# Optimization experiments

Hardware: AMD Instinct MI355X
Metric: run time of the kernel (lower is better)

The kernel has to match this reference:

```python
import jax, jax.numpy as jnp
import numpy as np

IN_FEATURES = 4096
OUT_FEATURES = 11008
GROUP_SIZE = 64
NUM_GROUPS = (OUT_FEATURES * IN_FEATURES) // GROUP_SIZE  # 704512, no padding


def setup_inputs() -> dict:
    key = jax.random.key(0)
    k_x, k_q, k_s, k_m, k_b = jax.random.split(key, 5)
    x = jax.random.normal(k_x, (2, 2048, IN_FEATURES), dtype=jnp.float32)
    weight_q3 = jax.random.randint(k_q, (NUM_GROUPS, GROUP_SIZE), 0, 8, dtype=jnp.int32)
    # positive scales, matching clamp(min=1e-8) in the quantizer
    weight_scales = jax.random.uniform(k_s, (NUM_GROUPS,), dtype=jnp.float32, minval=0.01, maxval=1.0)
    weight_sparse_mask = jax.random.uniform(k_m, (NUM_GROUPS, GROUP_SIZE)) < 0.1
    bias = jax.random.normal(k_b, (OUT_FEATURES,), dtype=jnp.float32)
    return {"x": x, "weight_q3": weight_q3, "weight_scales": weight_scales,
            "weight_sparse_mask": weight_sparse_mask, "bias": bias}


def _dequant(weight_q3, weight_scales, weight_sparse_mask):
    # x_norm = q/7; deq = x_norm*2*s - s = (2*q/7 - 1) * s ; masked -> 0
    scales = weight_scales[:, None]  # [G, 1]
    deq = (weight_q3.astype(jnp.float32) * (2.0 / 7.0) - 1.0) * scales
    deq = jnp.where(weight_sparse_mask, 0.0, deq)
    return deq.reshape(OUT_FEATURES, IN_FEATURES)


def reference(x, weight_q3, weight_scales, weight_sparse_mask, bias):
    W = _dequant(weight_q3, weight_scales, weight_sparse_mask)  # [O, I] fp32
    # F.linear: y = x @ W^T + b
    return jnp.einsum('bsi,oi->bso', x, W) + bias
```

## Files before the change

### kernel.cpp

```cpp
#include <hip/hip_runtime.h>
#include <hip/hip_bf16.h>

#define IN_F   4096
#define OUT_F  11008
#define MROWS  4096
#define BM     256
#define BN     256
#define BK     64
#define NT     (IN_F / BK)
#define CVT_CHUNKS (((long long)MROWS * IN_F) / 8)
#define TOT_CHUNKS (((long long)(MROWS + OUT_F) * IN_F) / 8)
#define PREP_GRID  2048

typedef __bf16 bf16x8 __attribute__((ext_vector_type(8)));
typedef float  f32x4  __attribute__((ext_vector_type(4)));

__global__ __launch_bounds__(256) void k_prep(const float* __restrict__ x,
                                              const int* __restrict__ q,
                                              const int* __restrict__ mask,
                                              const float* __restrict__ scales,
                                              __hip_bfloat16* __restrict__ xb,
                                              __hip_bfloat16* __restrict__ Wb)
{
    const long long stride = (long long)PREP_GRID * 256;
    for (long long c = (long long)blockIdx.x * 256 + threadIdx.x; c < TOT_CHUNKS; c += stride) {
        if (c < CVT_CHUNKS) {
            const long long base = c * 8;
            const float4 a = *(const float4*)(x + base);
            const float4 b = *(const float4*)(x + base + 4);
            float f[8] = {a.x, a.y, a.z, a.w, b.x, b.y, b.z, b.w};
            union { int4 v; __hip_bfloat16 h[8]; } u;
#pragma unroll
            for (int j = 0; j < 8; ++j) u.h[j] = __float2bfloat16(f[j]);
            *(int4*)(xb + base) = u.v;
        } else {
            const long long base = (c - CVT_CHUNKS) * 8;
            const int   g = (int)(base >> 6);
            const float s = scales[g];
            const int4 q0 = *(const int4*)(q + base);
            const int4 q1 = *(const int4*)(q + base + 4);
            const int4 m0 = *(const int4*)(mask + base);
            const int4 m1 = *(const int4*)(mask + base + 4);
            const float cc = 2.0f / 7.0f;
            int qa[8] = {q0.x, q0.y, q0.z, q0.w, q1.x, q1.y, q1.z, q1.w};
            int ma[8] = {m0.x, m0.y, m0.z, m0.w, m1.x, m1.y, m1.z, m1.w};
            union { int4 v; __hip_bfloat16 h[8]; } u;
#pragma unroll
            for (int j = 0; j < 8; ++j) {
                float w = ma[j] ? 0.0f : ((float)qa[j] * cc - 1.0f) * s;
                u.h[j] = __float2bfloat16(w);
            }
            *(int4*)(Wb + base) = u.v;
        }
    }
}

__device__ __forceinline__ void gl_lds16(const __hip_bfloat16* g, __hip_bfloat16* l)
{
    __builtin_amdgcn_global_load_lds(
        (const __attribute__((address_space(1))) void*)g,
        (__attribute__((address_space(3))) void*)l,
        16, 0, 0);
}

#define MMQ(IB, JB) do { \
    _Pragma("unroll") \
    for (int _jj = 0; _jj < 2; ++_jj) \
        _Pragma("unroll") \
        for (int _ii = 0; _ii < 4; ++_ii) \
            _Pragma("unroll") \
            for (int _kk = 0; _kk < 2; ++_kk) \
                acc[(IB) + _ii][(JB) + _jj] = __builtin_amdgcn_mfma_f32_16x16x32_bf16( \
                    bB[(JB) + _jj][_kk], bA[_ii][_kk], acc[(IB) + _ii][(JB) + _jj], 0, 0, 0); \
} while (0)

#define STAGE(gbase, ldsbase, k0, HF) do { \
    _Pragma("unroll") \
    for (int _t = 0; _t < 2; ++_t) { \
        const int _c = wave * 2 + _t; \
        const int _r = (HF) * 128 + _c * 8 + lrow; \
        gl_lds16((gbase) + (size_t)_r * IN_F + (k0) + lcol, (ldsbase) + _c * 512); \
    } \
} while (0)

#define TILE(BUF, T, SP1, SP2, VMODE, RD4) do { \
    const __hip_bfloat16* pA  = &As[(BUF)][0] + offA;         \
    const __hip_bfloat16* pB  = &Bs[(BUF)][0] + offB; \
    const __hip_bfloat16* pBn = &Bs[(BUF)^1][0] + offB; \
     \
    bA[0][0] = *(const bf16x8*)(pA + x0);        bA[0][1] = *(const bf16x8*)(pA + x1); \
    bA[1][0] = *(const bf16x8*)(pA + x0 + 2048); bA[1][1] = *(const bf16x8*)(pA + x1 + 2048); \
    bA[2][0] = *(const bf16x8*)(pA + x0 + 4096); bA[2][1] = *(const bf16x8*)(pA + x1 + 4096); \
    bA[3][0] = *(const bf16x8*)(pA + x0 + 6144); bA[3][1] = *(const bf16x8*)(pA + x1 + 6144); \
    if (SP1) STAGE(Bblk, &Bs[(BUF)^1][0], ((T)+1)*BK, 0); \
    __builtin_amdgcn_s_barrier(); \
    asm volatile("s_waitcnt lgkmcnt(0)" ::: "memory"); \
    __builtin_amdgcn_s_setprio(1); MMQ(0,0); __builtin_amdgcn_s_setprio(0); \
    __builtin_amdgcn_s_barrier(); \
     \
    bB[2][0] = *(const bf16x8*)(pB + x0 + 8192);  bB[2][1] = *(const bf16x8*)(pB + x1 + 8192); \
    bB[3][0] = *(const bf16x8*)(pB + x0 + 12288); bB[3][1] = *(const bf16x8*)(pB + x1 + 12288); \
    if (SP2) STAGE(Ablk, &As[(BUF)][0], ((T)+2)*BK, 0); \
    __builtin_amdgcn_s_barrier(); \
    asm volatile("s_waitcnt lgkmcnt(0)" ::: "memory"); \
    __builtin_amdgcn_s_setprio(1); MMQ(0,2); __builtin_amdgcn_s_setprio(0); \
    __builtin_amdgcn_s_barrier(); \
     \
    bA[0][0] = *(const bf16x8*)(pA + x0 + 8192);  bA[0][1] = *(const bf16x8*)(pA + x1 + 8192); \
    bA[1][0] = *(const bf16x8*)(pA + x0 + 10240); bA[1][1] = *(const bf16x8*)(pA + x1 + 10240); \
    bA[2][0] = *(const bf16x8*)(pA + x0 + 12288); bA[2][1] = *(const bf16x8*)(pA + x1 + 12288); \
    bA[3][0] = *(const bf16x8*)(pA + x0 + 14336); bA[3][1] = *(const bf16x8*)(pA + x1 + 14336); \
    if (SP2) STAGE(Bblk, &Bs[(BUF)][128*64], ((T)+2)*BK, 1); \
    __builtin_amdgcn_s_barrier(); \
    asm volatile("s_waitcnt lgkmcnt(0)" ::: "memory"); \
    __builtin_amdgcn_s_setprio(1); MMQ(4,0); __builtin_amdgcn_s_setprio(0); \
    __builtin_amdgcn_s_barrier(); \
     \
    if (SP2) STAGE(Ablk, &As[(BUF)][128*64], ((T)+2)*BK, 1); \
    __builtin_amdgcn_s_barrier(); \
    if ((VMODE) == 2)      asm volatile("s_waitcnt vmcnt(6)" ::: "memory"); \
    else if ((VMODE) == 1) asm volatile("s_waitcnt vmcnt(0)" ::: "memory"); \
    if (RD4) { \
        bB[0][0] = *(const bf16x8*)(pBn + x0);        bB[0][1] = *(const bf16x8*)(pBn + x1); \
        bB[1][0] = *(const bf16x8*)(pBn + x0 + 4096); bB[1][1] = *(const bf16x8*)(pBn + x1 + 4096); \
        __builtin_amdgcn_sched_barrier(0);   \
    } \
    __builtin_amdgcn_s_setprio(1); MMQ(4,2); __builtin_amdgcn_s_setprio(0); \
    __builtin_amdgcn_s_barrier(); \
} while (0)

__global__ __launch_bounds__(512, 2) void k_gemm(const __hip_bfloat16* __restrict__ A,
                                                 const __hip_bfloat16* __restrict__ B,
                                                 const float* __restrict__ bias,
                                                 float* __restrict__ C)
{
    __shared__ __align__(16) __hip_bfloat16 As[2][BM * BK];
    __shared__ __align__(16) __hip_bfloat16 Bs[2][BN * BK];

    const int tid  = threadIdx.x;
    const int lane = tid & 63;
    const int wave = tid >> 6;
    const int wm16 = (wave >> 2) * 16;
    const int wn16 = (wave & 3) * 16;
    const int quad = lane >> 4;
    const int lr   = lane & 15;
    const int swr  = lr & 7;
    const int lrow = lane >> 3;
    const int lcol = ((lane & 7) ^ lrow) * 8;

    const int offA = (wm16 + lr) * 64;
    const int offB = (wn16 + lr) * 64;
    const int x0   = (quad ^ swr) * 8;
    const int x1   = x0 ^ 32;

    const int orig = blockIdx.x;
    const int swz  = (orig & 7) * (688 >> 3) + (orig >> 3);
    const int bm   = swz & 15;
    const int bn   = swz >> 4;

    const __hip_bfloat16* Ablk = A + (size_t)bm * BM * IN_F;
    const __hip_bfloat16* Bblk = B + (size_t)bn * BN * IN_F;

    bf16x8 bA[4][2];
    bf16x8 bB[4][2];
    f32x4  acc[8][4];
#pragma unroll
    for (int i = 0; i < 8; ++i)
#pragma unroll
        for (int j = 0; j < 4; ++j)
            acc[i][j] = (f32x4){0.f, 0.f, 0.f, 0.f};

    STAGE(Bblk, &Bs[0][0],      0,  0);
    STAGE(Ablk, &As[0][0],      0,  0);
    STAGE(Bblk, &Bs[0][128*64], 0,  1);
    STAGE(Ablk, &As[0][128*64], 0,  1);
    STAGE(Ablk, &As[1][0],      BK, 0);
    STAGE(Bblk, &Bs[1][128*64], BK, 1);
    STAGE(Ablk, &As[1][128*64], BK, 1);
    asm volatile("s_waitcnt vmcnt(6)" ::: "memory");
    __builtin_amdgcn_s_barrier();
    {
        const __hip_bfloat16* pB0 = &Bs[0][0] + offB;
        bB[0][0] = *(const bf16x8*)(pB0 + x0);        bB[0][1] = *(const bf16x8*)(pB0 + x1);
        bB[1][0] = *(const bf16x8*)(pB0 + x0 + 4096); bB[1][1] = *(const bf16x8*)(pB0 + x1 + 4096);
    }

    for (int u = 0; u < (NT - 2) / 2; ++u) {
        const int t0 = 2 * u;
        TILE(0, t0,     1, 1, 2, 1);
        TILE(1, t0 + 1, 1, 1, 2, 1);
    }
    TILE(0, NT - 2, 1, 0, 1, 1);
    TILE(1, NT - 1, 0, 0, 0, 0);

#pragma unroll
    for (int j = 0; j < 4; ++j) {
        const int o = bn * BN + j * 64 + wn16 + quad * 4;
        const float4 bv = *(const float4*)(bias + o);
#pragma unroll
        for (int i = 0; i < 8; ++i) {
            const int s = bm * BM + i * 32 + wm16 + lr;
            float4 v;
            v.x = acc[i][j][0] + bv.x;
            v.y = acc[i][j][1] + bv.y;
            v.z = acc[i][j][2] + bv.z;
            v.w = acc[i][j][3] + bv.w;
            *(float4*)(C + (size_t)s * OUT_F + o) = v;
        }
    }
}

extern "C" void kernel_launch(void* const* d_in, const int* in_sizes, int n_in,
                              void* d_out, int out_size, void* d_ws, size_t ws_size,
                              hipStream_t stream)
{
    const float* x      = (const float*)d_in[0];
    const int*   q      = (const int*)d_in[1];
    const float* scales = (const float*)d_in[2];
    const int*   mask   = (const int*)d_in[3];
    const float* bias   = (const float*)d_in[4];
    float* out          = (float*)d_out;

    __hip_bfloat16* xb = (__hip_bfloat16*)d_ws;
    __hip_bfloat16* Wb = xb + (size_t)MROWS * IN_F;

    k_prep<<<PREP_GRID, 256, 0, stream>>>(x, q, mask, scales, xb, Wb);

    k_gemm<<<dim3(688), dim3(512), 0, stream>>>(xb, Wb, bias, out);
}
```

Measured before the change: 834.2 us.

## Stage full B tile two ahead and flatten prep into one-shot nontemporal blocks

The prep kernel drops its grid-stride loop and launches one 256-thread block per 1024 elements, with each thread converting 4 values through nontemporal vector loads. In the GEMM, the B sub-tile is now prefetched two K-steps ahead into the current buffer, like A, rather than one step ahead into the other buffer. The vmcnt wait moves to 8 and extra barriers and lgkmcnt waits are added to keep the LDS reuse safe. The extra barriers may add synchronisation stalls, and the prep kernel launches far more small blocks.

```diff
diff --git a/kernel.cpp b/kernel.cpp
--- a/kernel.cpp
+++ b/kernel.cpp
@@ -1,5 +1,6 @@
 #include <hip/hip_runtime.h>
 #include <hip/hip_bf16.h>
+
 
 #define IN_F   4096
 #define OUT_F  11008
@@ -8,12 +9,16 @@
 #define BN     256
 #define BK     64
 #define NT     (IN_F / BK)
-#define CVT_CHUNKS (((long long)MROWS * IN_F) / 8)
-#define TOT_CHUNKS (((long long)(MROWS + OUT_F) * IN_F) / 8)
-#define PREP_GRID  2048
+
+#define X_ELEMS ((long long)MROWS * IN_F)
+#define W_ELEMS ((long long)OUT_F * IN_F)
+#define XPREP_BLOCKS ((int)(X_ELEMS / (256 * 4)))
+#define WPREP_BLOCKS ((int)(W_ELEMS / (256 * 4)))
 
 typedef __bf16 bf16x8 __attribute__((ext_vector_type(8)));
 typedef float  f32x4  __attribute__((ext_vector_type(4)));
+typedef int    i32x4  __attribute__((ext_vector_type(4)));
+typedef unsigned int u32x2 __attribute__((ext_vector_type(2)));
 
 __global__ __launch_bounds__(256) void k_prep(const float* __restrict__ x,
                                               const int* __restrict__ q,
@@ -22,36 +27,28 @@
                                               __hip_bfloat16* __restrict__ xb,
                                               __hip_bfloat16* __restrict__ Wb)
 {
-    const long long stride = (long long)PREP_GRID * 256;
-    for (long long c = (long long)blockIdx.x * 256 + threadIdx.x; c < TOT_CHUNKS; c += stride) {
-        if (c < CVT_CHUNKS) {
-            const long long base = c * 8;
-            const float4 a = *(const float4*)(x + base);
-            const float4 b = *(const float4*)(x + base + 4);
-            float f[8] = {a.x, a.y, a.z, a.w, b.x, b.y, b.z, b.w};
-            union { int4 v; __hip_bfloat16 h[8]; } u;
-#pragma unroll
-            for (int j = 0; j < 8; ++j) u.h[j] = __float2bfloat16(f[j]);
-            *(int4*)(xb + base) = u.v;
-        } else {
-            const long long base = (c - CVT_CHUNKS) * 8;
-            const int   g = (int)(base >> 6);
-            const float s = scales[g];
-            const int4 q0 = *(const int4*)(q + base);
-            const int4 q1 = *(const int4*)(q + base + 4);
-            const int4 m0 = *(const int4*)(mask + base);
-            const int4 m1 = *(const int4*)(mask + base + 4);
-            const float cc = 2.0f / 7.0f;
-            int qa[8] = {q0.x, q0.y, q0.z, q0.w, q1.x, q1.y, q1.z, q1.w};
-            int ma[8] = {m0.x, m0.y, m0.z, m0.w, m1.x, m1.y, m1.z, m1.w};
-            union { int4 v; __hip_bfloat16 h[8]; } u;
-#pragma unroll
-            for (int j = 0; j < 8; ++j) {
-                float w = ma[j] ? 0.0f : ((float)qa[j] * cc - 1.0f) * s;
-                u.h[j] = __float2bfloat16(w);
-            }
-            *(int4*)(Wb + base) = u.v;
+    if (blockIdx.x < XPREP_BLOCKS) {
+        const long long t    = (long long)blockIdx.x * 256 + threadIdx.x;
+        const long long base = t * 4;
+        const f32x4 a = __builtin_nontemporal_load((const f32x4*)(x + base));
+        union { u32x2 v; __hip_bfloat16 h[4]; } u;
+#pragma unroll
+        for (int j = 0; j < 4; ++j) u.h[j] = __float2bfloat16(a[j]);
+        *(u32x2*)(xb + base) = u.v;
+    } else {
+        const long long t    = (long long)(blockIdx.x - XPREP_BLOCKS) * 256 + threadIdx.x;
+        const long long base = t * 4;
+        const float s  = scales[base >> 6];
+        const i32x4 qv = __builtin_nontemporal_load((const i32x4*)(q + base));
+        const i32x4 mv = __builtin_nontemporal_load((const i32x4*)(mask + base));
+        const float c = 2.0f / 7.0f;
+        union { u32x2 v; __hip_bfloat16 h[4]; } u;
+#pragma unroll
+        for (int j = 0; j < 4; ++j) {
+            float w = mv[j] ? 0.0f : ((float)qv[j] * c - 1.0f) * s;
+            u.h[j] = __float2bfloat16(w);
         }
+        *(u32x2*)(Wb + base) = u.v;
     }
 }
 
@@ -83,8 +80,8 @@
     } \
 } while (0)
 
-#define TILE(BUF, T, SP1, SP2, VMODE, RD4) do { \
-    const __hip_bfloat16* pA  = &As[(BUF)][0] + offA;         \
+#define TILE(BUF, T, SP, VMODE, RD4) do { \
+    const __hip_bfloat16* pA  = &As[(BUF)][0] + offA; \
     const __hip_bfloat16* pB  = &Bs[(BUF)][0] + offB; \
     const __hip_bfloat16* pBn = &Bs[(BUF)^1][0] + offB; \
      \
@@ -92,7 +89,7 @@
     bA[1][0] = *(const bf16x8*)(pA + x0 + 2048); bA[1][1] = *(const bf16x8*)(pA + x1 + 2048); \
     bA[2][0] = *(const bf16x8*)(pA + x0 + 4096); bA[2][1] = *(const bf16x8*)(pA + x1 + 4096); \
     bA[3][0] = *(const bf16x8*)(pA + x0 + 6144); bA[3][1] = *(const bf16x8*)(pA + x1 + 6144); \
-    if (SP1) STAGE(Bblk, &Bs[(BUF)^1][0], ((T)+1)*BK, 0); \
+    if (SP) STAGE(Bblk, &Bs[(BUF)][0], ((T)+2)*BK, 0); \
     __builtin_amdgcn_s_barrier(); \
     asm volatile("s_waitcnt lgkmcnt(0)" ::: "memory"); \
     __builtin_amdgcn_s_setprio(1); MMQ(0,0); __builtin_amdgcn_s_setprio(0); \
@@ -100,7 +97,7 @@
      \
     bB[2][0] = *(const bf16x8*)(pB + x0 + 8192);  bB[2][1] = *(const bf16x8*)(pB + x1 + 8192); \
     bB[3][0] = *(const bf16x8*)(pB + x0 + 12288); bB[3][1] = *(const bf16x8*)(pB + x1 + 12288); \
-    if (SP2) STAGE(Ablk, &As[(BUF)][0], ((T)+2)*BK, 0); \
+    if (SP) STAGE(Ablk, &As[(BUF)][0], ((T)+2)*BK, 0); \
     __builtin_amdgcn_s_barrier(); \
     asm volatile("s_waitcnt lgkmcnt(0)" ::: "memory"); \
     __builtin_amdgcn_s_setprio(1); MMQ(0,2); __builtin_amdgcn_s_setprio(0); \
@@ -110,22 +107,24 @@
     bA[1][0] = *(const bf16x8*)(pA + x0 + 10240); bA[1][1] = *(const bf16x8*)(pA + x1 + 10240); \
     bA[2][0] = *(const bf16x8*)(pA + x0 + 12288); bA[2][1] = *(const bf16x8*)(pA + x1 + 12288); \
     bA[3][0] = *(const bf16x8*)(pA + x0 + 14336); bA[3][1] = *(const bf16x8*)(pA + x1 + 14336); \
-    if (SP2) STAGE(Bblk, &Bs[(BUF)][128*64], ((T)+2)*BK, 1); \
+    if (SP) STAGE(Bblk, &Bs[(BUF)][128*64], ((T)+2)*BK, 1); \
     __builtin_amdgcn_s_barrier(); \
     asm volatile("s_waitcnt lgkmcnt(0)" ::: "memory"); \
     __builtin_amdgcn_s_setprio(1); MMQ(4,0); __builtin_amdgcn_s_setprio(0); \
     __builtin_amdgcn_s_barrier(); \
      \
-    if (SP2) STAGE(Ablk, &As[(BUF)][128*64], ((T)+2)*BK, 1); \
-    __builtin_amdgcn_s_barrier(); \
-    if ((VMODE) == 2)      asm volatile("s_waitcnt vmcnt(6)" ::: "memory"); \
+    if (SP) STAGE(Ablk, &As[(BUF)][128*64], ((T)+2)*BK, 1); \
+    __builtin_amdgcn_s_barrier(); \
+    if ((VMODE) == 2)      asm volatile("s_waitcnt vmcnt(8)" ::: "memory"); \
     else if ((VMODE) == 1) asm volatile("s_waitcnt vmcnt(0)" ::: "memory"); \
+    __builtin_amdgcn_s_barrier();    \
     if (RD4) { \
         bB[0][0] = *(const bf16x8*)(pBn + x0);        bB[0][1] = *(const bf16x8*)(pBn + x1); \
         bB[1][0] = *(const bf16x8*)(pBn + x0 + 4096); bB[1][1] = *(const bf16x8*)(pBn + x1 + 4096); \
         __builtin_amdgcn_sched_barrier(0);   \
     } \
     __builtin_amdgcn_s_setprio(1); MMQ(4,2); __builtin_amdgcn_s_setprio(0); \
+    if (RD4) asm volatile("s_waitcnt lgkmcnt(0)" ::: "memory");  \
     __builtin_amdgcn_s_barrier(); \
 } while (0)
 
@@ -174,38 +173,37 @@
     STAGE(Ablk, &As[0][0],      0,  0);
     STAGE(Bblk, &Bs[0][128*64], 0,  1);
     STAGE(Ablk, &As[0][128*64], 0,  1);
+    STAGE(Bblk, &Bs[1][0],      BK, 0);
     STAGE(Ablk, &As[1][0],      BK, 0);
     STAGE(Bblk, &Bs[1][128*64], BK, 1);
     STAGE(Ablk, &As[1][128*64], BK, 1);
-    asm volatile("s_waitcnt vmcnt(6)" ::: "memory");
+    asm volatile("s_waitcnt vmcnt(8)" ::: "memory");
     __builtin_amdgcn_s_barrier();
     {
         const __hip_bfloat16* pB0 = &Bs[0][0] + offB;
         bB[0][0] = *(const bf16x8*)(pB0 + x0);        bB[0][1] = *(const bf16x8*)(pB0 + x1);
         bB[1][0] = *(const bf16x8*)(pB0 + x0 + 4096); bB[1][1] = *(const bf16x8*)(pB0 + x1 + 4096);
     }
+    asm volatile("s_waitcnt lgkmcnt(0)" ::: "memory");
+    __builtin_amdgcn_s_barrier();
 
     for (int u = 0; u < (NT - 2) / 2; ++u) {
         const int t0 = 2 * u;
-        TILE(0, t0,     1, 1, 2, 1);
-        TILE(1, t0 + 1, 1, 1, 2, 1);
-    }
-    TILE(0, NT - 2, 1, 0, 1, 1);
-    TILE(1, NT - 1, 0, 0, 0, 0);
+        TILE(0, t0,     1, 2, 1);
+        TILE(1, t0 + 1, 1, 2, 1);
+    }
+    TILE(0, NT - 2, 0, 1, 1);
+    TILE(1, NT - 1, 0, 0, 0);
 
 #pragma unroll
     for (int j = 0; j < 4; ++j) {
         const int o = bn * BN + j * 64 + wn16 + quad * 4;
-        const float4 bv = *(const float4*)(bias + o);
+        const f32x4 bv = *(const f32x4*)(bias + o);
 #pragma unroll
         for (int i = 0; i < 8; ++i) {
             const int s = bm * BM + i * 32 + wm16 + lr;
-            float4 v;
-            v.x = acc[i][j][0] + bv.x;
-            v.y = acc[i][j][1] + bv.y;
-            v.z = acc[i][j][2] + bv.z;
-            v.w = acc[i][j][3] + bv.w;
-            *(float4*)(C + (size_t)s * OUT_F + o) = v;
+            f32x4 v = acc[i][j] + bv;
+            *(f32x4*)(C + (size_t)s * OUT_F + o) = v;
         }
     }
 }
@@ -224,7 +222,7 @@
     __hip_bfloat16* xb = (__hip_bfloat16*)d_ws;
     __hip_bfloat16* Wb = xb + (size_t)MROWS * IN_F;
 
-    k_prep<<<PREP_GRID, 256, 0, stream>>>(x, q, mask, scales, xb, Wb);
+    k_prep<<<XPREP_BLOCKS + WPREP_BLOCKS, 256, 0, stream>>>(x, q, mask, scales, xb, Wb);
 
     k_gemm<<<dim3(688), dim3(512), 0, stream>>>(xb, Wb, bias, out);
 }
```

After: 784.2 us. -6.0%, faster.
